# Kernel optimization log

Hardware: AMD Instinct MI355X
Metric: run time of the kernel (lower is better)

## Reference

```python
import jax, jax.numpy as jnp
import numpy as np

B, S, D, H, HD, KVH, FF = 2, 2048, 2048, 16, 128, 1, 8192
EPS = 1e-6
ROPE_BASE = 10000.0
NEG = -1e9


def _rms_norm(x, w):
    return x * jax.lax.rsqrt(jnp.mean(x * x, axis=-1, keepdims=True) + EPS) * w


def _rope(t):
    # t: [B, S, H, HD]; standard rotate-half RoPE
    half = HD // 2
    inv_freq = ROPE_BASE ** (-jnp.arange(0, HD, 2, dtype=jnp.float32) / HD)  # [half]
    ang = jnp.arange(S, dtype=jnp.float32)[:, None] * inv_freq               # [S, half]
    cos = jnp.concatenate([jnp.cos(ang), jnp.cos(ang)], axis=-1)[None, :, None, :]
    sin = jnp.concatenate([jnp.sin(ang), jnp.sin(ang)], axis=-1)[None, :, None, :]
    t1, t2 = t[..., :half], t[..., half:]
    rot = jnp.concatenate([-t2, t1], axis=-1)
    return t * cos + rot * sin


def _alibi_bias():
    # slopes for power-of-two head count: 2^(-8*(h+1)/H)
    slopes = 2.0 ** (-8.0 * (jnp.arange(H, dtype=jnp.float32) + 1.0) / H)    # [H]
    pos = jnp.arange(S, dtype=jnp.float32)
    dist = jnp.abs(pos[:, None] - pos[None, :])                              # [S, S]
    return (-slopes[:, None, None] * dist)[None]                             # [1, H, S, S]


def setup_inputs() -> dict:
    key = jax.random.key(0)
    ks = jax.random.split(key, 8)
    sc = lambda fan: 1.0 / np.sqrt(fan)
    x = jax.random.normal(ks[0], (B, S, D), jnp.float32)
    causal = jnp.where(jnp.tril(jnp.ones((S, S), bool)), 0.0, NEG).astype(jnp.float32)[None, None]
    return {
        "x": x,
        "mask": causal,                                                       # [1,1,S,S]
        "w_norm1": jnp.ones((D,), jnp.float32),
        "w_norm2": jnp.ones((D,), jnp.float32),
        "q_w": jax.random.normal(ks[1], (D, D), jnp.float32) * sc(D),        # [out,in] torch layout
        "kv_w": jax.random.normal(ks[2], (KVH * HD * 2, D), jnp.float32) * sc(D),
        "o_w": jax.random.normal(ks[3], (D, D), jnp.float32) * sc(D),
        "w1": jax.random.normal(ks[4], (FF, D), jnp.float32) * sc(D),
        "w2": jax.random.normal(ks[5], (FF, D), jnp.float32) * sc(D),
        "w3": jax.random.normal(ks[6], (D, FF), jnp.float32) * sc(FF),
    }


def reference(x, mask, w_norm1, w_norm2, q_w, kv_w, o_w, w1, w2, w3):
    # --- attention sub-block (pre-norm) ---
    h = _rms_norm(x, w_norm1)
    q = (h @ q_w.T).reshape(B, S, H, HD)                                      # [B,S,H,HD]
    kv = (h @ kv_w.T).reshape(B, S, KVH, 2, HD)
    k = jnp.broadcast_to(kv[:, :, :, 0, :], (B, S, H, HD))                    # MQA expand
    v = jnp.broadcast_to(kv[:, :, :, 1, :], (B, S, H, HD))
    q, k = _rope(q), _rope(k)
    scores = jnp.einsum('bshd,bthd->bhst', q, k) / np.sqrt(HD)                # [B,H,S,S]
    scores = scores + _alibi_bias() + mask
    attn = jax.nn.softmax(scores, axis=-1)
    out = jnp.einsum('bhst,bthd->bshd', attn, v).reshape(B, S, D)
    x = x + out @ o_w.T
    # --- SwiGLU FFN sub-block (pre-norm) ---
    h2 = _rms_norm(x, w_norm2)
    gated = jax.nn.silu(h2 @ w1.T) * (h2 @ w2.T)                              # [B,S,FF]
    return x + gated @ w3.T
```

## Files before the change

### kernel.cpp

```cpp
#include <hip/hip_runtime.h>
#include <stdint.h>

#define NB 2
#define NS 2048
#define ND 2048
#define NH 16
#define NHD 128
#define NFF 8192
#define NBS (NB*NS)
#define NQKV 2304

typedef unsigned short u16;
typedef __attribute__((ext_vector_type(8))) short bf16x8;
typedef __attribute__((ext_vector_type(4))) unsigned short u16x4;
typedef __attribute__((ext_vector_type(4))) float f32x4;

__device__ __forceinline__ u16 f2bf(float f) {
  union { float f; unsigned u; } v; v.f = f;
  unsigned r = v.u + 0x7fffu + ((v.u >> 16) & 1u);
  return (u16)(r >> 16);
}
__device__ __forceinline__ float bf2f(u16 h) {
  union { unsigned u; float f; } v; v.u = ((unsigned)h) << 16;
  return v.f;
}
__device__ __forceinline__ void async_cp16(const void* g, void* l) {
  __builtin_amdgcn_global_load_lds((const __attribute__((address_space(1))) void*)g,
                                   (__attribute__((address_space(3))) void*)l, 16, 0, 0);
}

__global__ void cvt_bf16_kernel(const float* __restrict__ in, u16* __restrict__ out, int n4) {
  int i = blockIdx.x * blockDim.x + threadIdx.x;
  if (i >= n4) return;
  float4 v = reinterpret_cast<const float4*>(in)[i];
  u16x4 o; o.x = f2bf(v.x); o.y = f2bf(v.y); o.z = f2bf(v.z); o.w = f2bf(v.w);
  reinterpret_cast<u16x4*>(out)[i] = o;
}

template <int BF16IN>
__global__ __launch_bounds__(256) void rmsnorm_kernel(const void* __restrict__ xin,
                                                      const float* __restrict__ w,
                                                      u16* __restrict__ out) {
  const int row = blockIdx.x, tid = threadIdx.x;
  float vs[8];
  if constexpr (BF16IN == 0) {
    const float* xr = (const float*)xin + (size_t)row * ND;
    float4 a = *reinterpret_cast<const float4*>(xr + tid * 8);
    float4 b = *reinterpret_cast<const float4*>(xr + tid * 8 + 4);
    vs[0]=a.x; vs[1]=a.y; vs[2]=a.z; vs[3]=a.w; vs[4]=b.x; vs[5]=b.y; vs[6]=b.z; vs[7]=b.w;
  } else {
    const u16* xr = (const u16*)xin + (size_t)row * ND;
    bf16x8 v = *reinterpret_cast<const bf16x8*>(xr + tid * 8);
#pragma unroll
    for (int j = 0; j < 8; ++j) vs[j] = bf2f((u16)v[j]);
  }
  float ss = 0.f;
#pragma unroll
  for (int j = 0; j < 8; ++j) ss += vs[j] * vs[j];
#pragma unroll
  for (int off = 32; off > 0; off >>= 1) ss += __shfl_down(ss, off);
  __shared__ float red[4];
  __shared__ float rinv_s;
  if ((tid & 63) == 0) red[tid >> 6] = ss;
  __syncthreads();
  if (tid == 0) rinv_s = rsqrtf((red[0] + red[1] + red[2] + red[3]) * (1.0f / ND) + 1e-6f);
  __syncthreads();
  const float rinv = rinv_s;
  const float* wr = w + tid * 8;
  u16* orow = out + (size_t)row * ND + tid * 8;
#pragma unroll
  for (int j = 0; j < 8; ++j) orow[j] = f2bf(vs[j] * rinv * wr[j]);
}

__global__ void rope_table_kernel(float* __restrict__ cosT, float* __restrict__ sinT) {
  int i = blockIdx.x * blockDim.x + threadIdx.x;
  if (i >= NS * 64) return;
  int s = i >> 6, d = i & 63;
  float freq = expf(-(float)d * (9.210340371976184f / 64.0f));
  float ang = (float)s * freq;
  cosT[i] = cosf(ang);
  sinT[i] = sinf(ang);
}

__global__ void rope_q_kernel(const u16* __restrict__ qkvraw, const float* __restrict__ cosT,
                              const float* __restrict__ sinT, u16* __restrict__ qout) {
  int i = blockIdx.x * blockDim.x + threadIdx.x;
  if (i >= NB * NS * NH * 64) return;
  int d = i & 63, h = (i >> 6) & 15, s = (i >> 10) & (NS - 1), b = i >> 21;
  size_t rrow = ((size_t)(b * NS + s)) * NQKV + h * NHD;
  float t1 = bf2f(qkvraw[rrow + d]);
  float t2 = bf2f(qkvraw[rrow + d + 64]);
  float c = cosT[(s << 6) + d], sn = sinT[(s << 6) + d];
  const float scale = 0.08838834764831845f;
  size_t orow = (((size_t)(b * NH + h)) * NS + s) * NHD;
  qout[orow + d]      = f2bf((t1 * c - t2 * sn) * scale);
  qout[orow + d + 64] = f2bf((t2 * c + t1 * sn) * scale);
}

__global__ void rope_kv_kernel(const u16* __restrict__ qkvraw, const float* __restrict__ cosT,
                               const float* __restrict__ sinT, u16* __restrict__ kout,
                               u16* __restrict__ vtout) {
  int i = blockIdx.x * blockDim.x + threadIdx.x;
  if (i >= NB * NS * 64) return;
  int d = i & 63, s = (i >> 6) & (NS - 1), b = i >> 17;
  size_t rrow = ((size_t)(b * NS + s)) * NQKV + ND;
  float t1 = bf2f(qkvraw[rrow + d]);
  float t2 = bf2f(qkvraw[rrow + d + 64]);
  float c = cosT[(s << 6) + d], sn = sinT[(s << 6) + d];
  size_t orow = ((size_t)(b * NS + s)) * NHD;
  kout[orow + d]      = f2bf(t1 * c - t2 * sn);
  kout[orow + d + 64] = f2bf(t2 * c + t1 * sn);
  vtout[((size_t)(b * 128 + d)) * NS + s]      = qkvraw[rrow + 128 + d];
  vtout[((size_t)(b * 128 + d + 64)) * NS + s] = qkvraw[rrow + 128 + d + 64];
}

template <int EPI>
__global__ __launch_bounds__(256) void gemm3_kernel(const u16* __restrict__ A,
                                                    const u16* __restrict__ W,
                                                    void* Out, const void* Aux,
                                                    int M, int N, int K) {
  __shared__ __align__(16) char As[128 * 128];
  __shared__ __align__(16) char Bs[128 * 128];
  const int tid = threadIdx.x, wave = tid >> 6, lane = tid & 63;
  const int lm = lane & 15, lg = lane >> 4;

  int bx, by;
  {
    const int gx = gridDim.x;
    if ((gx & 7) == 0) {
      const int id = blockIdx.y * gx + blockIdx.x;
      const int xcd = id & 7, rank = id >> 3;
      const int cw = gx >> 3;
      bx = xcd * cw + rank % cw;
      by = rank / cw;
    } else { bx = blockIdx.x; by = blockIdx.y; }
  }
  const int m0 = by * 128, n0 = bx * 128;
  const int wr = wave >> 1, wc = wave & 1;

  f32x4 acc[4][4];
#pragma unroll
  for (int i = 0; i < 4; ++i)
#pragma unroll
    for (int j = 0; j < 4; ++j) acc[i][j] = (f32x4){0.f, 0.f, 0.f, 0.f};

  for (int k0 = 0; k0 < K; k0 += 64) {
#pragma unroll
    for (int p = 0; p < 4; ++p) {
      int X = p * 4096 + tid * 16;
      int r = X >> 7;
      int sw = ((X >> 4) ^ (X >> 7)) & 7;
      async_cp16(A + (size_t)(m0 + r) * K + k0 + sw * 8, As + p * 4096 + wave * 1024);
      async_cp16(W + (size_t)(n0 + r) * K + k0 + sw * 8, Bs + p * 4096 + wave * 1024);
    }
    __syncthreads();
#pragma unroll
    for (int ks = 0; ks < 2; ++ks) {
      bf16x8 a[4], b[4];
#pragma unroll
      for (int i = 0; i < 4; ++i) {
        const int ra = wr * 64 + i * 16 + lm;
        const int sa = (ks * 4 + lg) ^ (ra & 7);
        a[i] = *(const bf16x8*)(As + ra * 128 + sa * 16);
        const int rb = wc * 64 + i * 16 + lm;
        const int sb = (ks * 4 + lg) ^ (rb & 7);
        b[i] = *(const bf16x8*)(Bs + rb * 128 + sb * 16);
      }
#pragma unroll
      for (int i = 0; i < 4; ++i)
#pragma unroll
        for (int j = 0; j < 4; ++j)
          acc[i][j] = __builtin_amdgcn_mfma_f32_16x16x32_bf16(a[i], b[j], acc[i][j], 0, 0, 0);
    }
    __syncthreads();
  }

#pragma unroll
  for (int i = 0; i < 4; ++i) {
    const int row_b = m0 + wr * 64 + i * 16 + lg * 4;
#pragma unroll
    for (int j = 0; j < 4; ++j) {
      const int col = n0 + wc * 64 + j * 16 + lm;
#pragma unroll
      for (int r = 0; r < 4; ++r) {
        size_t idx = (size_t)(row_b + r) * N + col;
        float v = acc[i][j][r];
        if constexpr (EPI == 0) {
          ((u16*)Out)[idx] = f2bf(v);
        } else if constexpr (EPI == 2) {
          float a1 = bf2f(((const u16*)Aux)[idx]);
          float s = a1 / (1.0f + expf(-a1));
          ((u16*)Out)[idx] = f2bf(s * v);
        } else if constexpr (EPI == 3) {
          ((u16*)Out)[idx] = f2bf(v + ((const float*)Aux)[idx]);
        } else {
          ((float*)Out)[idx] = v + bf2f(((const u16*)Aux)[idx]);
        }
      }
    }
  }
}

__global__ __launch_bounds__(512) void attn_kernel(const u16* __restrict__ q,
                                                   const u16* __restrict__ kg,
                                                   const u16* __restrict__ vt,
                                                   u16* __restrict__ out) {
  __shared__ __align__(16) u16 Klds[64 * 128];
  __shared__ __align__(16) u16 Vlds[128 * 64];
  __shared__ __align__(16) u16 Plds[8][16 * 72];
  const int tid = threadIdx.x, wave = tid >> 6, lane = tid & 63;
  const int bh = blockIdx.y, b = bh >> 4, h = bh & 15;
  const float slope = exp2f(-0.5f * (float)(h + 1));
  const int lm = lane & 15, lg = lane >> 4;
  const int crow = lg * 4;
  const int NT = NS / 128;
  u16* pw = Plds[wave];

#pragma unroll 1
  for (int half = 0; half < 2; ++half) {
    const int qt = half == 0 ? (NT - 1 - (int)blockIdx.x) : (int)blockIdx.x;
    const int q0 = qt * 128;

    bf16x8 qf[4];
    {
      const int qrow = q0 + wave * 16 + lm;
      const u16* qbase = q + ((size_t)bh * NS + qrow) * NHD + lg * 8;
#pragma unroll
      for (int kc = 0; kc < 4; ++kc) qf[kc] = *(const bf16x8*)(qbase + kc * 32);
    }

    float Mr[4], Lr[4];
    f32x4 O[8];
#pragma unroll
    for (int r = 0; r < 4; ++r) { Mr[r] = -__builtin_inff(); Lr[r] = 0.f; }
#pragma unroll
    for (int t = 0; t < 8; ++t) O[t] = (f32x4){0.f, 0.f, 0.f, 0.f};

    const int ntiles = 2 * qt + 2;
    for (int t0 = 0; t0 < ntiles; ++t0) {
      const int kv0 = t0 * 64;
      __syncthreads();
#pragma unroll
      for (int p = 0; p < 2; ++p) {
        int X = p * 8192 + tid * 16;
        int kv = X >> 8;
        int sl = (X >> 4) & 15;
        const u16* src = kg + ((size_t)b * NS + kv0 + kv) * NHD + ((sl ^ (kv & 7)) * 8);
        async_cp16(src, (char*)Klds + p * 8192 + wave * 1024);
      }
#pragma unroll
      for (int p = 0; p < 2; ++p) {
        int X = p * 8192 + tid * 16;
        int d = X >> 7;
        int sl = (X >> 4) & 7;
        const u16* src = vt + ((size_t)b * 128 + d) * NS + kv0 + ((sl ^ (d & 7)) * 8);
        async_cp16(src, (char*)Vlds + p * 8192 + wave * 1024);
      }
      __syncthreads();

      f32x4 sc[4];
#pragma unroll
      for (int sub = 0; sub < 4; ++sub) sc[sub] = (f32x4){0.f, 0.f, 0.f, 0.f};
#pragma unroll
      for (int sub = 0; sub < 4; ++sub) {
        const int kv = sub * 16 + lm;
#pragma unroll
        for (int kc = 0; kc < 4; ++kc) {
          const int slot = (kc * 4 + lg) ^ (kv & 7);
          bf16x8 kf = *(const bf16x8*)((const char*)Klds + kv * 256 + slot * 16);
          sc[sub] = __builtin_amdgcn_mfma_f32_16x16x32_bf16(qf[kc], kf, sc[sub], 0, 0, 0);
        }
      }

      float esc[4], pp[4][4];
#pragma unroll
      for (int r = 0; r < 4; ++r) {
        const int sq = q0 + wave * 16 + crow + r;
        float v[4];
#pragma unroll
        for (int sub = 0; sub < 4; ++sub) {
          const int kc_ = kv0 + sub * 16 + lm;
          v[sub] = (kc_ <= sq) ? sc[sub][r] - slope * (float)(sq - kc_) : -1e9f;
        }
        float mx = fmaxf(fmaxf(v[0], v[1]), fmaxf(v[2], v[3]));
        mx = fmaxf(mx, __shfl_xor(mx, 1));
        mx = fmaxf(mx, __shfl_xor(mx, 2));
        mx = fmaxf(mx, __shfl_xor(mx, 4));
        mx = fmaxf(mx, __shfl_xor(mx, 8));
        const float newM = fmaxf(Mr[r], mx);
        esc[r] = __expf(Mr[r] - newM);
        float rs = 0.f;
#pragma unroll
        for (int sub = 0; sub < 4; ++sub) { pp[sub][r] = __expf(v[sub] - newM); rs += pp[sub][r]; }
        rs += __shfl_xor(rs, 1);
        rs += __shfl_xor(rs, 2);
        rs += __shfl_xor(rs, 4);
        rs += __shfl_xor(rs, 8);
        Lr[r] = Lr[r] * esc[r] + rs;
        Mr[r] = newM;
      }
#pragma unroll
      for (int t = 0; t < 8; ++t) {
        O[t][0] *= esc[0]; O[t][1] *= esc[1]; O[t][2] *= esc[2]; O[t][3] *= esc[3];
      }

#pragma unroll
      for (int sub = 0; sub < 4; ++sub)
#pragma unroll
        for (int r = 0; r < 4; ++r)
          pw[(crow + r) * 72 + sub * 16 + lm] = f2bf(pp[sub][r]);

      bf16x8 pa0 = *(const bf16x8*)&pw[lm * 72 + lg * 8];
      bf16x8 pa1 = *(const bf16x8*)&pw[lm * 72 + 32 + lg * 8];

#pragma unroll
      for (int dt = 0; dt < 8; ++dt) {
        const int d = dt * 16 + lm;
        const int s0 = (lg) ^ (d & 7);
        const int s1 = (4 + lg) ^ (d & 7);
        bf16x8 vf0 = *(const bf16x8*)((const char*)Vlds + d * 128 + s0 * 16);
        bf16x8 vf1 = *(const bf16x8*)((const char*)Vlds + d * 128 + s1 * 16);
        O[dt] = __builtin_amdgcn_mfma_f32_16x16x32_bf16(pa0, vf0, O[dt], 0, 0, 0);
        O[dt] = __builtin_amdgcn_mfma_f32_16x16x32_bf16(pa1, vf1, O[dt], 0, 0, 0);
      }
    }

#pragma unroll
    for (int dt = 0; dt < 8; ++dt) {
#pragma unroll
      for (int r = 0; r < 4; ++r) {
        const int sq = q0 + wave * 16 + crow + r;
        out[((size_t)b * NS + sq) * ND + h * NHD + dt * 16 + lm] = f2bf(O[dt][r] / Lr[r]);
      }
    }
  }
}

extern "C" void kernel_launch(void* const* d_in, const int* in_sizes, int n_in,
                              void* d_out, int out_size, void* d_ws, size_t ws_size,
                              hipStream_t stream) {
  const float* x   = (const float*)d_in[0];
  const float* wn1 = (const float*)d_in[2];
  const float* wn2 = (const float*)d_in[3];
  const float* qw  = (const float*)d_in[4];
  const float* kvw = (const float*)d_in[5];
  const float* ow  = (const float*)d_in[6];
  const float* w1  = (const float*)d_in[7];
  const float* w2  = (const float*)d_in[8];
  const float* w3  = (const float*)d_in[9];
  float* out = (float*)d_out;

  const size_t MiB = 1024 * 1024;
  const size_t NEED = 161 * MiB;
  if (ws_size < NEED) return;

  char* ws = (char*)d_ws;
  u16*   WQKV   = (u16*)(ws);
  u16*   AO     = (u16*)(ws + 16 * MiB);
  u16*   OWB    = (u16*)(ws + 32 * MiB);
  u16*   W1B    = (u16*)(ws);
  u16*   W2B    = (u16*)(ws + 32 * MiB);
  u16*   W3B    = (u16*)(ws);
  u16*   QKVRAW = (u16*)(ws + 64 * MiB);
  u16*   A1     = (u16*)(ws + 64 * MiB);
  u16*   KB     = (u16*)(ws + 83 * MiB);
  u16*   VT     = (u16*)(ws + 84 * MiB);
  u16*   QB     = (u16*)(ws + 112 * MiB);
  u16*   X2B    = (u16*)(ws + 128 * MiB);
  u16*   Hbf    = (u16*)(ws + 144 * MiB);
  float* COS    = (float*)(ws + 160 * MiB);
  float* SIN    = (float*)(ws + 160 * MiB + 512 * 1024);

  auto cvt = [&](const float* src, u16* dst, size_t n) {
    int n4 = (int)(n / 4);
    cvt_bf16_kernel<<<(n4 + 255) / 256, 256, 0, stream>>>(src, dst, n4);
  };

  rope_table_kernel<<<(NS * 64 + 255) / 256, 256, 0, stream>>>(COS, SIN);

  rmsnorm_kernel<0><<<NBS, 256, 0, stream>>>(x, wn1, Hbf);

  cvt(qw, WQKV, (size_t)ND * ND);
  cvt(kvw, WQKV + (size_t)ND * ND, (size_t)256 * ND);
  gemm3_kernel<0><<<dim3(NQKV / 128, NBS / 128), 256, 0, stream>>>(
      Hbf, WQKV, (void*)QKVRAW, nullptr, NBS, NQKV, ND);

  rope_q_kernel<<<(NB * NS * NH * 64) / 256, 256, 0, stream>>>(QKVRAW, COS, SIN, QB);
  rope_kv_kernel<<<(NB * NS * 64) / 256, 256, 0, stream>>>(QKVRAW, COS, SIN, KB, VT);

  attn_kernel<<<dim3(NS / 256, NB * NH), 512, 0, stream>>>(QB, KB, VT, AO);

  cvt(ow, OWB, (size_t)ND * ND);
  gemm3_kernel<3><<<dim3(ND / 128, NBS / 128), 256, 0, stream>>>(
      AO, OWB, (void*)X2B, (const void*)x, NBS, ND, ND);

  rmsnorm_kernel<1><<<NBS, 256, 0, stream>>>(X2B, wn2, Hbf);

  cvt(w1, W1B, (size_t)NFF * ND);
  cvt(w2, W2B, (size_t)NFF * ND);
  gemm3_kernel<0><<<dim3(NFF / 128, NBS / 128), 256, 0, stream>>>(
      Hbf, W1B, (void*)A1, nullptr, NBS, NFF, ND);
  gemm3_kernel<2><<<dim3(NFF / 128, NBS / 128), 256, 0, stream>>>(
      Hbf, W2B, (void*)A1, (const void*)A1, NBS, NFF, ND);

  cvt(w3, W3B, (size_t)ND * NFF);
  gemm3_kernel<4><<<dim3(ND / 128, NBS / 128), 256, 0, stream>>>(
      A1, W3B, (void*)out, (const void*)X2B, NBS, ND, NFF);
}
```

Measured before the change: 800.7 us.

## Add 256x256 8-wave pipelined GEMM kernel for the W1 FFN projection

Adds a new GEMM kernel that uses 256x256 output tiles across 8 waves. It double-buffers LDS with async global-to-LDS loads split into half-K stages and swizzles LDS addresses to avoid bank conflicts. It interleaves MFMA bursts with the prefetch of the next tile, using explicit waitcnt, barriers and setprio, and remaps blocks by XCD. Only the h2@w1 GEMM is switched over; the goal is more data reuse per block and better overlap of loads with compute. The larger tiles mean fewer blocks and more register pressure.

```diff
diff --git a/kernel.cpp b/kernel.cpp
--- a/kernel.cpp
+++ b/kernel.cpp
@@ -27,6 +27,11 @@
 __device__ __forceinline__ void async_cp16(const void* g, void* l) {
   __builtin_amdgcn_global_load_lds((const __attribute__((address_space(1))) void*)g,
                                    (__attribute__((address_space(3))) void*)l, 16, 0, 0);
+}
+__device__ __forceinline__ void barrier_nofence() {
+  asm volatile("" ::: "memory");
+  __builtin_amdgcn_s_barrier();
+  asm volatile("" ::: "memory");
 }
 
 __global__ void cvt_bf16_kernel(const float* __restrict__ in, u16* __restrict__ out, int n4) {
@@ -196,6 +201,157 @@
         } else {
           ((float*)Out)[idx] = v + bf2f(((const u16*)Aux)[idx]);
         }
+      }
+    }
+  }
+}
+
+__global__ __launch_bounds__(512, 2) void gemm8p_kernel(const u16* __restrict__ A,
+                                                        const u16* __restrict__ W,
+                                                        u16* __restrict__ Out,
+                                                        int M, int N, int K) {
+  constexpr int HALF = 256 * 64;
+  __shared__ __align__(16) char As[2 * 2 * HALF];
+  __shared__ __align__(16) char Bs[2 * 2 * HALF];
+  const int tid = threadIdx.x, wave = tid >> 6, lane = tid & 63;
+  const int lm = lane & 15, lg = lane >> 4;
+
+  int bx, by;
+  {
+    const int gx = gridDim.x;
+    if ((gx & 7) == 0) {
+      const int id = blockIdx.y * gx + blockIdx.x;
+      const int xcd = id & 7, rank = id >> 3;
+      const int cw = gx >> 3;
+      bx = xcd * cw + rank % cw;
+      by = rank / cw;
+    } else { bx = blockIdx.x; by = blockIdx.y; }
+  }
+  const int m0 = by * 256, n0 = bx * 256;
+  const int wm = wave >> 2, wn = wave & 3;
+
+  f32x4 acc[8][4];
+#pragma unroll
+  for (int i = 0; i < 8; ++i)
+#pragma unroll
+    for (int j = 0; j < 4; ++j) acc[i][j] = (f32x4){0.f, 0.f, 0.f, 0.f};
+
+  const int nt = K >> 6;
+
+  auto stA = [&](int buf, int k0, int h) {
+#pragma unroll
+    for (int p = 0; p < 2; ++p) {
+      int idx = p * 512 + tid;
+      int r = idx >> 2, s = idx & 3;
+      int sg = s ^ (r & 3) ^ ((r >> 2) & 3);
+      async_cp16(A + (size_t)(m0 + r) * K + k0 + h * 32 + sg * 8,
+                 As + buf * (2 * HALF) + h * HALF + p * 8192 + wave * 1024);
+    }
+  };
+  auto stB = [&](int buf, int k0, int h) {
+#pragma unroll
+    for (int p = 0; p < 2; ++p) {
+      int idx = p * 512 + tid;
+      int r = idx >> 2, s = idx & 3;
+      int sg = s ^ (r & 3) ^ ((r >> 2) & 3);
+      async_cp16(W + (size_t)(n0 + r) * K + k0 + h * 32 + sg * 8,
+                 Bs + buf * (2 * HALF) + h * HALF + p * 8192 + wave * 1024);
+    }
+  };
+
+  bf16x8 a[4], b[4];
+  auto lda = [&](int buf, int mg, int ks) {
+#pragma unroll
+    for (int i = 0; i < 4; ++i) {
+      const int r = wm * 128 + mg * 64 + i * 16 + lm;
+      const int sl = lg ^ (r & 3) ^ ((r >> 2) & 3);
+      a[i] = *(const bf16x8*)(As + buf * (2 * HALF) + ks * HALF + r * 64 + sl * 16);
+    }
+  };
+  auto ldb = [&](int buf, int ks) {
+#pragma unroll
+    for (int j = 0; j < 4; ++j) {
+      const int r = wn * 64 + j * 16 + lm;
+      const int sl = lg ^ (r & 3) ^ ((r >> 2) & 3);
+      b[j] = *(const bf16x8*)(Bs + buf * (2 * HALF) + ks * HALF + r * 64 + sl * 16);
+    }
+  };
+
+#define SB __builtin_amdgcn_sched_barrier(0)
+#define LGKM0() do { asm volatile("s_waitcnt lgkmcnt(0)" ::: "memory"); SB; } while (0)
+#define MM(MB)                                                          \
+  do {                                                                  \
+    __builtin_amdgcn_s_setprio(1);                                      \
+    _Pragma("unroll")                                                   \
+    for (int i = 0; i < 4; ++i)                                         \
+      _Pragma("unroll")                                                 \
+      for (int j = 0; j < 4; ++j)                                       \
+        acc[(MB) + i][j] = __builtin_amdgcn_mfma_f32_16x16x32_bf16(     \
+            a[i], b[j], acc[(MB) + i][j], 0, 0, 0);                     \
+    __builtin_amdgcn_s_setprio(0);                                      \
+    SB;                                                                 \
+  } while (0)
+
+  stA(0, 0, 0); stB(0, 0, 0); stA(0, 0, 1); stB(0, 0, 1);
+  asm volatile("s_waitcnt vmcnt(0)" ::: "memory");
+  SB;
+  barrier_nofence();
+
+  for (int t = 0; t < nt; ++t) {
+    const int cur = t & 1, nb = cur ^ 1;
+    const bool pf = (t + 1 < nt);
+    const int nk = (t + 1) << 6;
+
+    lda(cur, 0, 0); ldb(cur, 0);
+    if (pf) stA(nb, nk, 0);
+    SB;
+    barrier_nofence();
+    LGKM0();
+    MM(0);
+    barrier_nofence();
+
+    lda(cur, 1, 0);
+    if (pf) stB(nb, nk, 0);
+    SB;
+    barrier_nofence();
+    LGKM0();
+    MM(4);
+    if (pf) asm volatile("s_waitcnt vmcnt(4)" ::: "memory");
+    else    asm volatile("s_waitcnt vmcnt(0)" ::: "memory");
+    SB;
+    barrier_nofence();
+
+    lda(cur, 1, 1); ldb(cur, 1);
+    if (pf) stA(nb, nk, 1);
+    SB;
+    barrier_nofence();
+    LGKM0();
+    MM(4);
+    barrier_nofence();
+
+    lda(cur, 0, 1);
+    if (pf) stB(nb, nk, 1);
+    SB;
+    barrier_nofence();
+    LGKM0();
+    MM(0);
+    if (pf) { asm volatile("s_waitcnt vmcnt(4)" ::: "memory"); SB; }
+    barrier_nofence();
+  }
+#undef MM
+#undef LGKM0
+#undef SB
+
+#pragma unroll
+  for (int i = 0; i < 8; ++i) {
+    const int row_b = m0 + wm * 128 + i * 16 + lg * 4;
+#pragma unroll
+    for (int j = 0; j < 4; ++j) {
+      const int col = n0 + wn * 64 + j * 16 + lm;
+#pragma unroll
+      for (int r = 0; r < 4; ++r) {
+        size_t idx = (size_t)(row_b + r) * N + col;
+        Out[idx] = f2bf(acc[i][j][r]);
       }
     }
   }
@@ -398,8 +554,8 @@
 
   cvt(w1, W1B, (size_t)NFF * ND);
   cvt(w2, W2B, (size_t)NFF * ND);
-  gemm3_kernel<0><<<dim3(NFF / 128, NBS / 128), 256, 0, stream>>>(
-      Hbf, W1B, (void*)A1, nullptr, NBS, NFF, ND);
+  gemm8p_kernel<<<dim3(NFF / 256, NBS / 256), 512, 0, stream>>>(
+      Hbf, W1B, A1, NBS, NFF, ND);
   gemm3_kernel<2><<<dim3(NFF / 128, NBS / 128), 256, 0, stream>>>(
       Hbf, W2B, (void*)A1, (const void*)A1, NBS, NFF, ND);
 
```

Result: no change. 788.3 us, median of 2 (-1.6%).
